# Kernel tuning notes

Measured on AMD Instinct MI355X. Metric: run time of the kernel, lower is better.

## Reference

```python
import jax, jax.numpy as jnp
import numpy as np

B, N, C = 16, 1024, 768
E, H, D, K = 8, 192, 4, 2


def setup_inputs() -> dict:
    key = jax.random.key(0)
    ks = jax.random.split(key, 8)
    std = 0.02
    return {
        "x": jax.random.normal(ks[0], (B, N, C), jnp.float32),
        "task_ids": jax.random.randint(ks[1], (B,), 0, D),
        "eps": jax.random.normal(ks[2], (B, N, E), jnp.float32),
        "gate_w": jax.random.normal(ks[3], (D, C, 2 * E), jnp.float32) * std,
        "fc1_w": jax.random.normal(ks[4], (E, H, C), jnp.float32) * std,
        "fc1_b": jnp.zeros((E, H), jnp.float32),
        "fc2_w": jax.random.normal(ks[5], (E, C, H), jnp.float32) * std,
        "fc2_b": jnp.zeros((E, C), jnp.float32),
    }


def reference(x, task_ids, eps, gate_w, fc1_w, fc1_b, fc2_w, fc2_b):
    # per-sample gate selected by domain/task id: [B,N,2E]
    total_w = jnp.einsum("bnc,bce->bne", x, gate_w[task_ids])
    clean_logits, raw_noise = jnp.split(total_w, 2, axis=-1)  # [B,N,E] each
    noise_stddev = jax.nn.softplus(raw_noise) + 0.01
    logits = clean_logits + eps * noise_stddev  # [B,N,E]
    exp_wise_sum = logits.sum(axis=1)  # [B,E]

    top_k_logits, top_k_idx = jax.lax.top_k(exp_wise_sum, K)  # [B,K]
    m1 = top_k_logits.min(axis=1, keepdims=True)
    m2 = top_k_logits.max(axis=1, keepdims=True)
    scaled = (top_k_logits - m1) / (m2 - m1 + 1e-6)
    top_k_gates = jax.nn.softmax(scaled, axis=1)  # [B,K]

    gates_full = jnp.zeros((B, E), x.dtype).at[
        jnp.arange(B)[:, None], top_k_idx
    ].set(top_k_gates)  # [B,E]

    # dense all-expert adapter compute (faithful to original torch.stack)
    h = jnp.einsum("bnc,ehc->benh", x, fc1_w) + fc1_b[None, :, None, :]
    h = jax.nn.gelu(h, approximate=False)
    expert_outs = jnp.einsum("benh,ech->benc", h, fc2_w) + fc2_b[None, :, None, :]

    tot_x = jnp.einsum("be,benc->bnc", gates_full, expert_outs)
    return x + tot_x
```

## Files before the change

kernel.cpp:

```cpp
#include <hip/hip_runtime.h>

#define B_ 16
#define N_ 1024
#define C_ 768
#define E_ 8
#define H_ 192

typedef __bf16 bf16x8 __attribute__((ext_vector_type(8)));
typedef float  f32x4  __attribute__((ext_vector_type(4)));

__global__ __launch_bounds__(256) void prep_kernel(
    const float* __restrict__ w1, const float* __restrict__ w2,
    const float* __restrict__ gw,
    __bf16* __restrict__ pw1, __bf16* __restrict__ pw2,
    float* __restrict__ gwT) {
  int idx = blockIdx.x * 256 + threadIdx.x;
  const int nW4 = (E_ * H_ * C_) / 4;
  if (idx >= nW4) return;
  int flat = idx * 4;
  int e = flat / (H_ * C_);
  int r = flat - e * (H_ * C_);

  {
    float4 a = *(const float4*)(w1 + (size_t)flat);
    int n = r / C_;
    int c = r - n * C_;
    size_t o = ((size_t)(e * 24 + (c >> 5)) * 192 + n) * 32 + (c & 31);
    pw1[o + 0] = (__bf16)a.x; pw1[o + 1] = (__bf16)a.y;
    pw1[o + 2] = (__bf16)a.z; pw1[o + 3] = (__bf16)a.w;
  }
  {
    float4 a = *(const float4*)(w2 + (size_t)flat);
    int n = r / H_;
    int h = r - n * H_;
    size_t o = ((size_t)(e * 6 + (h >> 5)) * 768 + n) * 32 + (h & 31);
    pw2[o + 0] = (__bf16)a.x; pw2[o + 1] = (__bf16)a.y;
    pw2[o + 2] = (__bf16)a.z; pw2[o + 3] = (__bf16)a.w;
  }
  if (idx < (4 * 16 * C_) / 4) {
    int f = idx * 4;
    int d = f / (16 * C_);
    int rr = f - d * (16 * C_);
    int j = rr / C_;
    int c = rr - j * C_;
    const float* src = gw + (size_t)d * C_ * 16 + j;
    float4 v;
    v.x = src[(size_t)(c + 0) * 16]; v.y = src[(size_t)(c + 1) * 16];
    v.z = src[(size_t)(c + 2) * 16]; v.w = src[(size_t)(c + 3) * 16];
    *(float4*)(gwT + (size_t)f) = v;
  }
}

__global__ __launch_bounds__(256, 3) void gate_kernel(
    const float* __restrict__ x, const int* __restrict__ task_ids,
    const float* __restrict__ eps, const float* __restrict__ gwT,
    float* __restrict__ psums) {
  const int b = blockIdx.x >> 6;
  const int token0 = (blockIdx.x & 63) * 16;
  const int tid = threadIdx.x;

  __shared__ __align__(16) float xt[16][772];
  __shared__ float sc[16][16];
  __shared__ float red[16][8];

  const float* xbase = x + ((size_t)b * N_ + token0) * C_;
  for (int it = 0; it < 12; ++it) {
    int chunk = it * 256 + tid;
    int row = chunk / 192;
    int col4 = chunk - row * 192;
    float4 v = *(const float4*)(xbase + (size_t)row * C_ + col4 * 4);
    *(float4*)&xt[row][col4 * 4] = v;
  }
  __syncthreads();

  const int t = tid & 15;
  const int j = tid >> 4;
  const int task = task_ids[b];
  const float* wrow = gwT + ((size_t)task * 16 + j) * C_;
  float acc = 0.0f;
#pragma unroll 4
  for (int c = 0; c < C_; c += 4) {
    float4 xv = *(const float4*)&xt[t][c];
    float4 wv = *(const float4*)(wrow + c);
    acc += xv.x * wv.x + xv.y * wv.y + xv.z * wv.z + xv.w * wv.w;
  }
  sc[t][j] = acc;
  __syncthreads();
  if (j < 8) {
    float clean = sc[t][j];
    float raw = sc[t][j + 8];
    float sp = (raw > 20.0f) ? raw : log1pf(expf(raw));
    red[t][j] = clean +
        eps[((size_t)b * N_ + token0 + t) * E_ + j] * (sp + 0.01f);
  }
  __syncthreads();
  if (tid < 8) {
    float s = 0.0f;
#pragma unroll
    for (int tt = 0; tt < 16; ++tt) s += red[tt][tid];
    psums[(size_t)blockIdx.x * 8 + tid] = s;
  }
}

#define SMEM_EXPERT (64 * 776 * 2 + 64 * 200 * 2 + 32)

__global__ __launch_bounds__(768, 3) void expert_kernel(
    const float* __restrict__ x, const __bf16* __restrict__ pw1,
    const __bf16* __restrict__ pw2, const float* __restrict__ fc1_b,
    const float* __restrict__ fc2_b, const float* __restrict__ psums,
    float* __restrict__ out) {
  const int bid = blockIdx.x;
  const int sxc = bid >> 3;
  const int b = (bid & 7) * 2 + (sxc >> 4);
  const int token0 = (sxc & 15) * 64;
  const int tid = threadIdx.x;
  const int wave = tid >> 6;
  const int wm = wave / 6;
  const int wn = wave - wm * 6;
  const int lane = tid & 63;
  const int ln = lane & 15;
  const int q8 = (lane >> 4) * 8;
  const int q4 = (lane >> 4) * 4;
  const int arow = wm * 32;

  extern __shared__ char smem[];
  __bf16 (*xs)[776] = reinterpret_cast<__bf16(*)[776]>(smem);
  __bf16 (*hs)[200] = reinterpret_cast<__bf16(*)[200]>(smem + 99328);
  float* smc = reinterpret_cast<float*>(smem + 99328 + 25600);

  if (wave < 8) {
    float v = psums[(((size_t)b << 6) | lane) * 8 + wave];
#pragma unroll
    for (int off = 32; off; off >>= 1) v += __shfl_down(v, off);
    if (lane == 0) smc[wave] = v;
  }
  __syncthreads();

  int e_idx[2]; float gate_v[2];
  {
    float best = -INFINITY, best2 = -INFINITY;
    int i1 = 0, i2 = 0;
#pragma unroll
    for (int e = 0; e < E_; ++e) {
      float v = smc[e];
      if (v > best) { best2 = best; i2 = i1; best = v; i1 = e; }
      else if (v > best2) { best2 = v; i2 = e; }
    }
    float d = best - best2;
    float st = d / (d + 1e-6f);
    float et = expf(st);
    e_idx[0] = i1; gate_v[0] = et / (et + 1.0f);
    e_idx[1] = i2; gate_v[1] = 1.0f / (et + 1.0f);
  }

  bf16x8 bq[3][2];
  {
    const __bf16* w1l = pw1 + (size_t)e_idx[0] * (24 * 192 * 32)
                            + (size_t)(wn * 32 + ln) * 32 + q8;
#pragma unroll
    for (int k0 = 0; k0 < 3; ++k0)
#pragma unroll
      for (int jj = 0; jj < 2; ++jj)
        bq[k0][jj] = *(const bf16x8*)(w1l + (size_t)k0 * 6144 + jj * 512);
  }

  const float* xbase = x + ((size_t)b * N_ + token0) * C_;
  for (int it = 0; it < 8; ++it) {
    int chunk = it * 768 + tid;
    int row = chunk / 96;
    int col8 = chunk - row * 96;
    const float* p = xbase + (size_t)row * C_ + col8 * 8;
    float4 v0 = *(const float4*)p;
    float4 v1 = *(const float4*)(p + 4);
    bf16x8 tv;
    tv[0] = (__bf16)v0.x; tv[1] = (__bf16)v0.y; tv[2] = (__bf16)v0.z; tv[3] = (__bf16)v0.w;
    tv[4] = (__bf16)v1.x; tv[5] = (__bf16)v1.y; tv[6] = (__bf16)v1.z; tv[7] = (__bf16)v1.w;
    *(bf16x8*)&xs[row][col8 * 8] = tv;
  }
  __syncthreads();

  f32x4 c2[2][8] = {};

  for (int kx = 0; kx < 2; ++kx) {
    const int e = e_idx[kx];
    const float g = gate_v[kx];

    const __bf16* w1l = pw1 + (size_t)e * (24 * 192 * 32)
                            + (size_t)(wn * 32 + ln) * 32 + q8;
    if (kx == 1) {
#pragma unroll
      for (int k0 = 0; k0 < 3; ++k0)
#pragma unroll
        for (int jj = 0; jj < 2; ++jj)
          bq[k0][jj] = *(const bf16x8*)(w1l + (size_t)k0 * 6144 + jj * 512);
    }
    bf16x8 aq[3][2];
#pragma unroll
    for (int k0 = 0; k0 < 3; ++k0) {
      aq[k0][0] = *(const bf16x8*)&xs[arow + ln][k0 * 32 + q8];
      aq[k0][1] = *(const bf16x8*)&xs[arow + 16 + ln][k0 * 32 + q8];
    }
    f32x4 c1[2][2] = {};
#pragma unroll
    for (int kb = 0; kb < 24; ++kb) {
      const int p = kb % 3;
#pragma unroll
      for (int jj = 0; jj < 2; ++jj) {
        c1[0][jj] = __builtin_amdgcn_mfma_f32_16x16x32_bf16(aq[p][0], bq[p][jj], c1[0][jj], 0, 0, 0);
        c1[1][jj] = __builtin_amdgcn_mfma_f32_16x16x32_bf16(aq[p][1], bq[p][jj], c1[1][jj], 0, 0, 0);
      }
      if (kb < 21) {
        const int kn = kb + 3;
        const __bf16* nx = w1l + (size_t)kn * 6144;
#pragma unroll
        for (int jj = 0; jj < 2; ++jj) bq[p][jj] = *(const bf16x8*)(nx + jj * 512);
        aq[p][0] = *(const bf16x8*)&xs[arow + ln][kn * 32 + q8];
        aq[p][1] = *(const bf16x8*)&xs[arow + 16 + ln][kn * 32 + q8];
      }
    }
#pragma unroll
    for (int jj = 0; jj < 2; ++jj) {
      int col = wn * 32 + jj * 16 + ln;
      float b1 = fc1_b[e * H_ + col];
#pragma unroll
      for (int m = 0; m < 2; ++m) {
#pragma unroll
        for (int r = 0; r < 4; ++r) {
          int row = arow + m * 16 + q4 + r;
          float v = c1[m][jj][r] + b1;
          float gl = 0.5f * v * (1.0f + erff(v * 0.70710678118f));
          hs[row][col] = (__bf16)(g * gl);
        }
      }
    }
    __syncthreads();

#pragma unroll
    for (int pass = 0; pass < 2; ++pass) {
      const __bf16* w2l = pw2 + (size_t)e * (6 * 768 * 32)
                              + (size_t)(wn * 128 + pass * 64 + ln) * 32 + q8;
      bf16x8 bh[2][4], av[2][2];
#pragma unroll
      for (int jj = 0; jj < 4; ++jj) bh[0][jj] = *(const bf16x8*)(w2l + jj * 512);
      av[0][0] = *(const bf16x8*)&hs[arow + ln][q8];
      av[0][1] = *(const bf16x8*)&hs[arow + 16 + ln][q8];
#pragma unroll
      for (int kb = 0; kb < 6; ++kb) {
        const int p = kb & 1;
        if (kb < 5) {
          const __bf16* src = w2l + (size_t)(kb + 1) * 24576;
#pragma unroll
          for (int jj = 0; jj < 4; ++jj)
            bh[p ^ 1][jj] = *(const bf16x8*)(src + jj * 512);
          av[p ^ 1][0] = *(const bf16x8*)&hs[arow + ln][(kb + 1) * 32 + q8];
          av[p ^ 1][1] = *(const bf16x8*)&hs[arow + 16 + ln][(kb + 1) * 32 + q8];
        }
#pragma unroll
        for (int jj = 0; jj < 4; ++jj) {
          const int cj = pass * 4 + jj;
          c2[0][cj] = __builtin_amdgcn_mfma_f32_16x16x32_bf16(av[p][0], bh[p][jj], c2[0][cj], 0, 0, 0);
          c2[1][cj] = __builtin_amdgcn_mfma_f32_16x16x32_bf16(av[p][1], bh[p][jj], c2[1][cj], 0, 0, 0);
        }
      }
    }
    __syncthreads();
  }

  const float* xr = x + ((size_t)b * N_ + token0) * C_;
  float* outr = out + ((size_t)b * N_ + token0) * C_;
#pragma unroll
  for (int jj = 0; jj < 8; ++jj) {
    int col = wn * 128 + jj * 16 + ln;
    float b2t = gate_v[0] * fc2_b[e_idx[0] * C_ + col] +
                gate_v[1] * fc2_b[e_idx[1] * C_ + col];
#pragma unroll
    for (int m = 0; m < 2; ++m) {
#pragma unroll
      for (int r = 0; r < 4; ++r) {
        int row = arow + m * 16 + q4 + r;
        size_t off = (size_t)row * C_ + col;
        outr[off] = xr[off] + c2[m][jj][r] + b2t;
      }
    }
  }
}

extern "C" void kernel_launch(void* const* d_in, const int* in_sizes, int n_in,
                              void* d_out, int out_size, void* d_ws, size_t ws_size,
                              hipStream_t stream) {
  const float* x      = (const float*)d_in[0];
  const int*   task   = (const int*)d_in[1];
  const float* eps    = (const float*)d_in[2];
  const float* gate_w = (const float*)d_in[3];
  const float* fc1_w  = (const float*)d_in[4];
  const float* fc1_b  = (const float*)d_in[5];
  const float* fc2_w  = (const float*)d_in[6];
  const float* fc2_b  = (const float*)d_in[7];
  float* out = (float*)d_out;

  const size_t nW = (size_t)E_ * H_ * C_;
  __bf16* pw1 = (__bf16*)d_ws;
  __bf16* pw2 = pw1 + nW;
  float* gwT   = (float*)((char*)d_ws + 2 * nW * sizeof(__bf16));
  float* psums = gwT + 4 * 16 * C_;

  prep_kernel<<<(nW / 4 + 255) / 256, 256, 0, stream>>>(fc1_w, fc2_w, gate_w,
                                                        pw1, pw2, gwT);
  gate_kernel<<<B_ * 64, 256, 0, stream>>>(x, task, eps, gwT, psums);

  hipFuncSetAttribute(reinterpret_cast<const void*>(expert_kernel),
                      hipFuncAttributeMaxDynamicSharedMemorySize, SMEM_EXPERT);
  expert_kernel<<<B_ * 16, 768, SMEM_EXPERT, stream>>>(
      x, pw1, pw2, fc1_b, fc2_b, psums, out);
}
```

Baseline: 205.6 us.

## Fuse gate and expert kernels into one cooperative kernel with grid sync

Merges the gating kernel into the expert kernel. Each block now loads its 64-token x tile once, computing both the fp32 gate logits and the bf16 copy used by the expert GEMMs, writes per-block partial sums, and then waits on a cooperative grid-wide sync before reading the per-batch sums. This removes one kernel launch and a second full read of x. In exchange it relies on all 256 blocks being co-resident, adds a grid barrier, and makes the gate compute run inside large 768-thread blocks, where it may use the hardware less well than the old separate kernel did.

```diff
diff --git a/kernel.cpp b/kernel.cpp
--- a/kernel.cpp
+++ b/kernel.cpp
@@ -1,4 +1,7 @@
 #include <hip/hip_runtime.h>
+#include <hip/hip_cooperative_groups.h>
+
+namespace cg = cooperative_groups;
 
 #define B_ 16
 #define N_ 1024
@@ -7,6 +10,7 @@
 #define H_ 192
 
 typedef __bf16 bf16x8 __attribute__((ext_vector_type(8)));
+typedef __bf16 bf16x4 __attribute__((ext_vector_type(4)));
 typedef float  f32x4  __attribute__((ext_vector_type(4)));
 
 __global__ __launch_bounds__(256) void prep_kernel(
@@ -51,64 +55,20 @@
   }
 }
 
-__global__ __launch_bounds__(256, 3) void gate_kernel(
+#define XS_OFF   0
+#define XF_OFF   99328
+#define HS_OFF   99328
+#define SC_OFF   (99328 + 49408)
+#define RED_OFF  (SC_OFF + 3072)
+#define BS_OFF   (RED_OFF + 512)
+#define SMEM_FUSED (BS_OFF + 64)
+
+__global__ __launch_bounds__(768, 3) void fused_kernel(
     const float* __restrict__ x, const int* __restrict__ task_ids,
     const float* __restrict__ eps, const float* __restrict__ gwT,
-    float* __restrict__ psums) {
-  const int b = blockIdx.x >> 6;
-  const int token0 = (blockIdx.x & 63) * 16;
-  const int tid = threadIdx.x;
-
-  __shared__ __align__(16) float xt[16][772];
-  __shared__ float sc[16][16];
-  __shared__ float red[16][8];
-
-  const float* xbase = x + ((size_t)b * N_ + token0) * C_;
-  for (int it = 0; it < 12; ++it) {
-    int chunk = it * 256 + tid;
-    int row = chunk / 192;
-    int col4 = chunk - row * 192;
-    float4 v = *(const float4*)(xbase + (size_t)row * C_ + col4 * 4);
-    *(float4*)&xt[row][col4 * 4] = v;
-  }
-  __syncthreads();
-
-  const int t = tid & 15;
-  const int j = tid >> 4;
-  const int task = task_ids[b];
-  const float* wrow = gwT + ((size_t)task * 16 + j) * C_;
-  float acc = 0.0f;
-#pragma unroll 4
-  for (int c = 0; c < C_; c += 4) {
-    float4 xv = *(const float4*)&xt[t][c];
-    float4 wv = *(const float4*)(wrow + c);
-    acc += xv.x * wv.x + xv.y * wv.y + xv.z * wv.z + xv.w * wv.w;
-  }
-  sc[t][j] = acc;
-  __syncthreads();
-  if (j < 8) {
-    float clean = sc[t][j];
-    float raw = sc[t][j + 8];
-    float sp = (raw > 20.0f) ? raw : log1pf(expf(raw));
-    red[t][j] = clean +
-        eps[((size_t)b * N_ + token0 + t) * E_ + j] * (sp + 0.01f);
-  }
-  __syncthreads();
-  if (tid < 8) {
-    float s = 0.0f;
-#pragma unroll
-    for (int tt = 0; tt < 16; ++tt) s += red[tt][tid];
-    psums[(size_t)blockIdx.x * 8 + tid] = s;
-  }
-}
-
-#define SMEM_EXPERT (64 * 776 * 2 + 64 * 200 * 2 + 32)
-
-__global__ __launch_bounds__(768, 3) void expert_kernel(
-    const float* __restrict__ x, const __bf16* __restrict__ pw1,
-    const __bf16* __restrict__ pw2, const float* __restrict__ fc1_b,
-    const float* __restrict__ fc2_b, const float* __restrict__ psums,
-    float* __restrict__ out) {
+    const __bf16* __restrict__ pw1, const __bf16* __restrict__ pw2,
+    const float* __restrict__ fc1_b, const float* __restrict__ fc2_b,
+    float* __restrict__ psums, float* __restrict__ out) {
   const int bid = blockIdx.x;
   const int sxc = bid >> 3;
   const int b = (bid & 7) * 2 + (sxc >> 4);
@@ -122,17 +82,81 @@
   const int q8 = (lane >> 4) * 8;
   const int q4 = (lane >> 4) * 4;
   const int arow = wm * 32;
+  const int task = task_ids[b];
 
   extern __shared__ char smem[];
-  __bf16 (*xs)[776] = reinterpret_cast<__bf16(*)[776]>(smem);
-  __bf16 (*hs)[200] = reinterpret_cast<__bf16(*)[200]>(smem + 99328);
-  float* smc = reinterpret_cast<float*>(smem + 99328 + 25600);
-
-  if (wave < 8) {
-    float v = psums[(((size_t)b << 6) | lane) * 8 + wave];
-#pragma unroll
-    for (int off = 32; off; off >>= 1) v += __shfl_down(v, off);
-    if (lane == 0) smc[wave] = v;
+  __bf16 (*xs)[776] = reinterpret_cast<__bf16(*)[776]>(smem + XS_OFF);
+  float  (*xf)[772] = reinterpret_cast<float(*)[772]>(smem + XF_OFF);
+  __bf16 (*hs)[200] = reinterpret_cast<__bf16(*)[200]>(smem + HS_OFF);
+  float (*sc)[16][3] = reinterpret_cast<float(*)[16][3]>(smem + SC_OFF);
+  float (*red)[8] = reinterpret_cast<float(*)[8]>(smem + RED_OFF);
+  float* bsum = reinterpret_cast<float*>(smem + BS_OFF);
+  float* smc  = bsum + 8;
+
+  if (tid < 8) bsum[tid] = 0.0f;
+
+  const float* xbase = x + ((size_t)b * N_ + token0) * C_;
+  for (int g = 0; g < 4; ++g) {
+    for (int it = 0; it < 4; ++it) {
+      int chunk = it * 768 + tid;
+      int row = chunk / 192;
+      int col4 = (chunk - row * 192) * 4;
+      float4 v = *(const float4*)(xbase + ((size_t)(g * 16 + row)) * C_ + col4);
+      *(float4*)&xf[row][col4] = v;
+      bf16x4 o;
+      o[0] = (__bf16)v.x; o[1] = (__bf16)v.y; o[2] = (__bf16)v.z; o[3] = (__bf16)v.w;
+      *(bf16x4*)&xs[g * 16 + row][col4] = o;
+    }
+    __syncthreads();
+
+    {
+      const int ck = tid >> 8;
+      const int vt = tid & 255;
+      const int t = vt & 15;
+      const int j = vt >> 4;
+      const float* wr = gwT + ((size_t)task * 16 + j) * C_ + ck * 256;
+      const float* xr_ = &xf[t][ck * 256];
+      float acc = 0.0f;
+#pragma unroll 4
+      for (int c = 0; c < 256; c += 4) {
+        f32x4 xv = *(const f32x4*)(xr_ + c);
+        f32x4 wv = *(const f32x4*)(wr + c);
+        acc += xv[0] * wv[0] + xv[1] * wv[1] + xv[2] * wv[2] + xv[3] * wv[3];
+      }
+      sc[t][j][ck] = acc;
+    }
+    __syncthreads();
+
+    if (tid < 128) {
+      int t = tid >> 3, e2 = tid & 7;
+      float clean = sc[t][e2][0] + sc[t][e2][1] + sc[t][e2][2];
+      float raw   = sc[t][e2 + 8][0] + sc[t][e2 + 8][1] + sc[t][e2 + 8][2];
+      float sp = (raw > 20.0f) ? raw : log1pf(expf(raw));
+      red[t][e2] = clean +
+          eps[((size_t)b * N_ + token0 + g * 16 + t) * E_ + e2] * (sp + 0.01f);
+    }
+    __syncthreads();
+    if (tid < 8) {
+      float s = bsum[tid];
+#pragma unroll
+      for (int t = 0; t < 16; ++t) s += red[t][tid];
+      bsum[tid] = s;
+    }
+    __syncthreads();
+  }
+  if (tid < 8) psums[bid * 8 + tid] = bsum[tid];
+  __threadfence();
+
+  cg::this_grid().sync();
+
+  if (tid < 8) {
+    float s = 0.0f;
+#pragma unroll
+    for (int tile = 0; tile < 16; ++tile) {
+      int srcbid = (((b & 1) * 16 + tile) << 3) | (b >> 1);
+      s += psums[srcbid * 8 + tid];
+    }
+    smc[tid] = s;
   }
   __syncthreads();
 
@@ -163,21 +187,6 @@
       for (int jj = 0; jj < 2; ++jj)
         bq[k0][jj] = *(const bf16x8*)(w1l + (size_t)k0 * 6144 + jj * 512);
   }
-
-  const float* xbase = x + ((size_t)b * N_ + token0) * C_;
-  for (int it = 0; it < 8; ++it) {
-    int chunk = it * 768 + tid;
-    int row = chunk / 96;
-    int col8 = chunk - row * 96;
-    const float* p = xbase + (size_t)row * C_ + col8 * 8;
-    float4 v0 = *(const float4*)p;
-    float4 v1 = *(const float4*)(p + 4);
-    bf16x8 tv;
-    tv[0] = (__bf16)v0.x; tv[1] = (__bf16)v0.y; tv[2] = (__bf16)v0.z; tv[3] = (__bf16)v0.w;
-    tv[4] = (__bf16)v1.x; tv[5] = (__bf16)v1.y; tv[6] = (__bf16)v1.z; tv[7] = (__bf16)v1.w;
-    *(bf16x8*)&xs[row][col8 * 8] = tv;
-  }
-  __syncthreads();
 
   f32x4 c2[2][8] = {};
 
@@ -306,10 +315,13 @@
 
   prep_kernel<<<(nW / 4 + 255) / 256, 256, 0, stream>>>(fc1_w, fc2_w, gate_w,
                                                         pw1, pw2, gwT);
-  gate_kernel<<<B_ * 64, 256, 0, stream>>>(x, task, eps, gwT, psums);
-
-  hipFuncSetAttribute(reinterpret_cast<const void*>(expert_kernel),
-                      hipFuncAttributeMaxDynamicSharedMemorySize, SMEM_EXPERT);
-  expert_kernel<<<B_ * 16, 768, SMEM_EXPERT, stream>>>(
-      x, pw1, pw2, fc1_b, fc2_b, psums, out);
+
+  hipFuncSetAttribute(reinterpret_cast<const void*>(fused_kernel),
+                      hipFuncAttributeMaxDynamicSharedMemorySize, SMEM_FUSED);
+  void* args[] = {(void*)&x, (void*)&task, (void*)&eps, (void*)&gwT,
+                  (void*)&pw1, (void*)&pw2, (void*)&fc1_b, (void*)&fc2_b,
+                  (void*)&psums, (void*)&out};
+  hipLaunchCooperativeKernel(reinterpret_cast<void*>(fused_kernel),
+                             dim3(B_ * 16), dim3(768), args, SMEM_FUSED,
+                             stream);
 }
```

Result: slower. 294.6 us (+43.3%).
